# Optimization experiments

Measured on AMD Instinct MI355X. Metric: run time of the kernel, lower is better.

Reference implementation:

```python
import jax, jax.numpy as jnp
import numpy as np

B, N, DIM, H = 8, 1024, 1024, 16
D = DIM // H  # head dim = 64
SCALE = DIM ** (-0.5)  # NOTE: original uses full dim, not head dim


def setup_inputs() -> dict:
    key = jax.random.key(0)
    ks = jax.random.split(key, 8)
    x = jax.random.normal(ks[0], (B, N, DIM), dtype=jnp.float32)
    pos = jax.random.normal(ks[1], (B, N, DIM), dtype=jnp.float32)
    mask = jax.random.bernoulli(ks[2], 0.9, (B, N - 1))  # bool, [b, n-1]
    w_std = 0.02
    W_qk = jax.random.normal(ks[3], (2 * DIM, DIM), dtype=jnp.float32) * w_std  # Linear(dim, 2*dim_qk)
    W_v = jax.random.normal(ks[4], (DIM, DIM), dtype=jnp.float32) * w_std
    W_out = jax.random.normal(ks[5], (DIM, DIM), dtype=jnp.float32) * w_std
    b_out = jax.random.normal(ks[6], (DIM,), dtype=jnp.float32) * w_std
    return {"x": x, "mask": mask, "pos": pos, "W_qk": W_qk, "W_v": W_v,
            "W_out": W_out, "b_out": b_out}


def _split_heads(t):
    # b n (h d) -> b h n d
    b, n, _ = t.shape
    return t.reshape(b, n, H, D).transpose(0, 2, 1, 3)


def reference(x, mask, pos, W_qk, W_v, W_out, b_out):
    qk = x @ W_qk.T                       # [b, n, 2*dim]
    q, k = jnp.split(qk, 2, axis=-1)
    v = x @ W_v.T                         # [b, n, dim]
    q, k, v = _split_heads(q), _split_heads(k), _split_heads(v)  # [b,h,n,d]
    hpos = _split_heads(pos)
    q = q + hpos
    k = k + hpos
    dots = jnp.einsum('bhid,bhjd->bhij', q, k) * SCALE  # [b,h,n,n]
    mask_value = -jnp.finfo(dots.dtype).max
    # pad mask with True at position 0 (CLS token always visible)
    m = jnp.pad(mask, ((0, 0), (1, 0)), constant_values=True)  # [b, n]
    m2 = m[:, None, :] & m[:, :, None]                          # [b, n, n]
    dots = jnp.where(m2[:, None, :, :], dots, mask_value)
    attn = jax.nn.softmax(dots, axis=-1)
    out = jnp.einsum('bhij,bhjd->bhid', attn, v)  # [b,h,n,d]
    out = out.transpose(0, 2, 1, 3).reshape(x.shape[0], x.shape[1], DIM)  # b n (h d)
    out = out @ W_out.T + b_out  # dropout p=0.0 -> identity
    return out
```

## Files before the change

### kernel.cpp

```cpp
#include <hip/hip_runtime.h>


typedef unsigned short u16;
typedef short bf16x8 __attribute__((ext_vector_type(8)));
typedef float f32x4 __attribute__((ext_vector_type(4)));
typedef float f32x16 __attribute__((ext_vector_type(16)));

#define MFMA16(a, b, c) __builtin_amdgcn_mfma_f32_16x16x32_bf16((a), (b), (c), 0, 0, 0)
#define MFMA32(a, b, c) __builtin_amdgcn_mfma_f32_32x32x16_bf16((a), (b), (c), 0, 0, 0)

__device__ __forceinline__ u16 f2bf(float f) {
    union { float f; unsigned u; } x; x.f = f;
    unsigned r = x.u + 0x7fffu + ((x.u >> 16) & 1u);
    return (u16)(r >> 16);
}

__device__ __forceinline__ void gld16(const u16* g, u16* l) {
    __builtin_amdgcn_global_load_lds(
        (const __attribute__((address_space(1))) void*)g,
        (__attribute__((address_space(3))) void*)l, 16, 0, 0);
}

__global__ __launch_bounds__(256) void cast_f32_bf16(const float* __restrict__ src,
                                                     u16* __restrict__ dst, int n4) {
    int i = blockIdx.x * 256 + threadIdx.x;
    if (i < n4) {
        float4 v = ((const float4*)src)[i];
        ushort4 o;
        o.x = f2bf(v.x); o.y = f2bf(v.y); o.z = f2bf(v.z); o.w = f2bf(v.w);
        ((ushort4*)dst)[i] = o;
    }
}

__global__ __launch_bounds__(256) void gemm_qk(
    const u16* __restrict__ A,
    const u16* __restrict__ Bw,
    const float* __restrict__ pos,
    u16* __restrict__ Q, u16* __restrict__ Kx) {
    const int n0 = blockIdx.x * 128, m0 = blockIdx.y * 128;
    const int t = threadIdx.x, w = t >> 6, ln = t & 63;
    const int l15 = ln & 15, l4 = ln >> 4;
    const int wm = (w >> 1) * 64, wn = (w & 1) * 64;

    __shared__ u16 As[128 * 64];
    __shared__ u16 Bs[128 * 64];

    f32x4 acc[4][4];
#pragma unroll
    for (int i = 0; i < 4; ++i)
#pragma unroll
        for (int j = 0; j < 4; ++j) acc[i][j] = (f32x4){0.f, 0.f, 0.f, 0.f};

    const int sr = ln >> 3;
    const int scx = ((ln & 7) ^ sr) * 8;
    const int x0 = (l15 & 7);
    for (int k0 = 0; k0 < 1024; k0 += 64) {
        __syncthreads();
#pragma unroll
        for (int p = 0; p < 4; ++p) {
            int rbase = w * 32 + p * 8;
            gld16(A  + (size_t)(m0 + rbase + sr) * 1024 + k0 + scx, &As[rbase * 64]);
            gld16(Bw + (size_t)(n0 + rbase + sr) * 1024 + k0 + scx, &Bs[rbase * 64]);
        }
        __syncthreads();
#pragma unroll
        for (int kt = 0; kt < 2; ++kt) {
            bf16x8 a[4], bfr[4];
#pragma unroll
            for (int mt = 0; mt < 4; ++mt)
                a[mt] = *(const bf16x8*)&As[(wm + mt * 16 + l15) * 64 + ((kt * 4 + l4) ^ x0) * 8];
#pragma unroll
            for (int nt = 0; nt < 4; ++nt)
                bfr[nt] = *(const bf16x8*)&Bs[(wn + nt * 16 + l15) * 64 + ((kt * 4 + l4) ^ x0) * 8];
#pragma unroll
            for (int mt = 0; mt < 4; ++mt)
#pragma unroll
                for (int nt = 0; nt < 4; ++nt)
                    acc[mt][nt] = MFMA16(a[mt], bfr[nt], acc[mt][nt]);
        }
    }
#pragma unroll
    for (int mt = 0; mt < 4; ++mt)
#pragma unroll
        for (int nt = 0; nt < 4; ++nt)
#pragma unroll
            for (int r = 0; r < 4; ++r) {
                int i = m0 + wm + mt * 16 + l4 * 4 + r;
                int j = n0 + wn + nt * 16 + l15;
                int bb = i >> 10, n = i & 1023;
                int jj = j & 1023;
                float v = acc[mt][nt][r] + pos[(size_t)i * 1024 + jj];
                int hh = jj >> 6, dd = jj & 63;
                size_t idx = (((size_t)(bb * 16 + hh)) * 1024 + n) * 64 + dd;
                if (j < 1024) Q[idx] = f2bf(v * 0.045084220027780106f);
                else          Kx[idx] = f2bf(v);
            }
}

__global__ __launch_bounds__(256) void gemm_v(
    const u16* __restrict__ Wv,
    const u16* __restrict__ X,
    u16* __restrict__ Vt) {
    const int n0 = blockIdx.x * 128, m0 = blockIdx.y * 128;
    const int bIdx = blockIdx.z;
    const u16* Xb = X + (size_t)bIdx * 1048576;
    const int t = threadIdx.x, w = t >> 6, ln = t & 63;
    const int l15 = ln & 15, l4 = ln >> 4;
    const int wm = (w >> 1) * 64, wn = (w & 1) * 64;

    __shared__ u16 As[128 * 64];
    __shared__ u16 Bs[128 * 64];

    f32x4 acc[4][4];
#pragma unroll
    for (int i = 0; i < 4; ++i)
#pragma unroll
        for (int j = 0; j < 4; ++j) acc[i][j] = (f32x4){0.f, 0.f, 0.f, 0.f};

    const int sr = ln >> 3;
    const int scx = ((ln & 7) ^ sr) * 8;
    const int x0 = (l15 & 7);
    for (int k0 = 0; k0 < 1024; k0 += 64) {
        __syncthreads();
#pragma unroll
        for (int p = 0; p < 4; ++p) {
            int rbase = w * 32 + p * 8;
            gld16(Wv + (size_t)(m0 + rbase + sr) * 1024 + k0 + scx, &As[rbase * 64]);
            gld16(Xb + (size_t)(n0 + rbase + sr) * 1024 + k0 + scx, &Bs[rbase * 64]);
        }
        __syncthreads();
#pragma unroll
        for (int kt = 0; kt < 2; ++kt) {
            bf16x8 a[4], bfr[4];
#pragma unroll
            for (int mt = 0; mt < 4; ++mt)
                a[mt] = *(const bf16x8*)&As[(wm + mt * 16 + l15) * 64 + ((kt * 4 + l4) ^ x0) * 8];
#pragma unroll
            for (int nt = 0; nt < 4; ++nt)
                bfr[nt] = *(const bf16x8*)&Bs[(wn + nt * 16 + l15) * 64 + ((kt * 4 + l4) ^ x0) * 8];
#pragma unroll
            for (int mt = 0; mt < 4; ++mt)
#pragma unroll
                for (int nt = 0; nt < 4; ++nt)
                    acc[mt][nt] = MFMA16(a[mt], bfr[nt], acc[mt][nt]);
        }
    }
#pragma unroll
    for (int mt = 0; mt < 4; ++mt)
#pragma unroll
        for (int nt = 0; nt < 4; ++nt)
#pragma unroll
            for (int r = 0; r < 4; ++r) {
                int i = m0 + wm + mt * 16 + l4 * 4 + r;
                int j = n0 + wn + nt * 16 + l15;
                Vt[((size_t)(bIdx * 1024 + i)) * 1024 + j] = f2bf(acc[mt][nt][r]);
            }
}

__global__ __launch_bounds__(64) void vsum_kernel(const u16* __restrict__ Vt,
                                                  float* __restrict__ Vsum) {
    int row = blockIdx.x, ln = threadIdx.x;
    const u16* p = Vt + (size_t)row * 1024 + ln * 16;
    uint4 a = *(const uint4*)p;
    uint4 bq = *(const uint4*)(p + 8);
    float s = 0.f;
    unsigned vv[8] = {a.x, a.y, a.z, a.w, bq.x, bq.y, bq.z, bq.w};
#pragma unroll
    for (int i = 0; i < 8; ++i) {
        s += __uint_as_float(vv[i] << 16);
        s += __uint_as_float(vv[i] & 0xffff0000u);
    }
#pragma unroll
    for (int d = 1; d < 64; d <<= 1) s += __shfl_xor(s, d);
    if (ln == 0) Vsum[row] = s;
}

__global__ __launch_bounds__(256) void attn_kernel(
    const u16* __restrict__ Q,
    const u16* __restrict__ Kx,
    const u16* __restrict__ Vt,
    const int* __restrict__ maskIn,
    const float* __restrict__ Vsum,
    u16* __restrict__ O) {
    const int gid = blockIdx.x;
    const int bh = gid & 127;
    const int qt = gid >> 7;
    const int b = bh >> 4, h = bh & 15;
    const int t = threadIdx.x, w = t >> 6, ln = t & 63;
    const int l31 = ln & 31, l5 = ln >> 5;

    __shared__ u16 Ks[64 * 72];
    __shared__ u16 Vs[64 * 72];
    __shared__ float cvf[64];

    const size_t qkbase = (size_t)bh * 65536;
    const int q0 = qt * 128 + w * 32;
    const int q = q0 + l31;

    bf16x8 bq[4];
#pragma unroll
    for (int kt = 0; kt < 4; ++kt)
        bq[kt] = *(const bf16x8*)(Q + qkbase + (size_t)q * 64 + kt * 16 + l5 * 8);

    const bool rqv = (q == 0) || (maskIn[b * 1023 + q - 1] != 0);

    float lsum = 0.f;
    f32x16 o0 = {0,0,0,0,0,0,0,0,0,0,0,0,0,0,0,0};
    f32x16 o1 = {0,0,0,0,0,0,0,0,0,0,0,0,0,0,0,0};

    const int srow = t >> 2, sc = (t & 3) * 16;

    for (int j0 = 0; j0 < 1024; j0 += 64) {
        __syncthreads();
        {
            uint4 kv = *(const uint4*)(Kx + qkbase + (size_t)(j0 + srow) * 64 + sc);
            uint4 kv2 = *(const uint4*)(Kx + qkbase + (size_t)(j0 + srow) * 64 + sc + 8);
            *(uint4*)&Ks[srow * 72 + sc] = kv;
            *(uint4*)&Ks[srow * 72 + sc + 8] = kv2;
            uint4 vv = *(const uint4*)(Vt + (size_t)bh * 65536 + (size_t)srow * 1024 + j0 + sc);
            uint4 vv2 = *(const uint4*)(Vt + (size_t)bh * 65536 + (size_t)srow * 1024 + j0 + sc + 8);
            *(uint4*)&Vs[srow * 72 + sc] = vv;
            *(uint4*)&Vs[srow * 72 + sc + 8] = vv2;
            if (t < 64) {
                int kk = j0 + t;
                bool cv = (kk == 0) || (maskIn[b * 1023 + kk - 1] != 0);
                cvf[t] = cv ? 0.f : -1e30f;
            }
        }
        __syncthreads();

        f32x16 st0 = {0,0,0,0,0,0,0,0,0,0,0,0,0,0,0,0};
        f32x16 st1 = {0,0,0,0,0,0,0,0,0,0,0,0,0,0,0,0};
#pragma unroll
        for (int ktk = 0; ktk < 4; ++ktk) {
            bf16x8 ak0 = *(const bf16x8*)&Ks[(l31) * 72 + ktk * 16 + l5 * 8];
            bf16x8 ak1 = *(const bf16x8*)&Ks[(32 + l31) * 72 + ktk * 16 + l5 * 8];
            st0 = MFMA32(ak0, bq[ktk], st0);
            st1 = MFMA32(ak1, bq[ktk], st1);
        }
#pragma unroll
        for (int g = 0; g < 4; ++g) {
            f32x4 cv0 = *(const f32x4*)&cvf[g * 8 + l5 * 4];
            f32x4 cv1 = *(const f32x4*)&cvf[32 + g * 8 + l5 * 4];
#pragma unroll
            for (int r = 0; r < 4; ++r) {
                float p0 = __builtin_amdgcn_exp2f(st0[g * 4 + r] + cv0[r]);
                float p1 = __builtin_amdgcn_exp2f(st1[g * 4 + r] + cv1[r]);
                st0[g * 4 + r] = p0;
                st1[g * 4 + r] = p1;
                lsum += p0 + p1;
            }
        }
        unsigned pk0[8], pk1[8];
#pragma unroll
        for (int g = 0; g < 4; ++g) {
#pragma unroll
            for (int qq = 0; qq < 2; ++qq) {
                unsigned a0 = __float_as_uint(st0[g * 4 + 2 * qq]) + 0x8000u;
                unsigned a1 = __float_as_uint(st0[g * 4 + 2 * qq + 1]) + 0x8000u;
                pk0[2 * g + qq] = (a1 & 0xffff0000u) | (a0 >> 16);
                unsigned c0 = __float_as_uint(st1[g * 4 + 2 * qq]) + 0x8000u;
                unsigned c1 = __float_as_uint(st1[g * 4 + 2 * qq + 1]) + 0x8000u;
                pk1[2 * g + qq] = (c1 & 0xffff0000u) | (c0 >> 16);
            }
        }
        bf16x8 pf[4];
#pragma unroll
        for (int kt = 0; kt < 4; ++kt) {
            const int hh = kt & 1;
            unsigned own0, own1, off0, off1;
            if (kt < 2) {
                own0 = l5 ? pk0[4 * hh + 2] : pk0[4 * hh];
                own1 = l5 ? pk0[4 * hh + 3] : pk0[4 * hh + 1];
                off0 = l5 ? pk0[4 * hh]     : pk0[4 * hh + 2];
                off1 = l5 ? pk0[4 * hh + 1] : pk0[4 * hh + 3];
            } else {
                own0 = l5 ? pk1[4 * hh + 2] : pk1[4 * hh];
                own1 = l5 ? pk1[4 * hh + 3] : pk1[4 * hh + 1];
                off0 = l5 ? pk1[4 * hh]     : pk1[4 * hh + 2];
                off1 = l5 ? pk1[4 * hh + 1] : pk1[4 * hh + 3];
            }
            unsigned ex0 = (unsigned)__shfl_xor((int)off0, 32);
            unsigned ex1 = (unsigned)__shfl_xor((int)off1, 32);
            unsigned dw0 = l5 ? ex0 : own0;
            unsigned dw1 = l5 ? ex1 : own1;
            unsigned dw2 = l5 ? own0 : ex0;
            unsigned dw3 = l5 ? own1 : ex1;
            union { unsigned u[4]; bf16x8 v; } cv;
            cv.u[0] = dw0; cv.u[1] = dw1; cv.u[2] = dw2; cv.u[3] = dw3;
            pf[kt] = cv.v;
        }
#pragma unroll
        for (int kt = 0; kt < 4; ++kt) {
            bf16x8 av0 = *(const bf16x8*)&Vs[(l31) * 72 + kt * 16 + l5 * 8];
            bf16x8 av1 = *(const bf16x8*)&Vs[(32 + l31) * 72 + kt * 16 + l5 * 8];
            o0 = MFMA32(av0, pf[kt], o0);
            o1 = MFMA32(av1, pf[kt], o1);
        }
    }
    float lrow = lsum + __shfl_xor(lsum, 32);
    const float linv = 1.f / lrow;
    const int n = q0 + l31;
    u16* orow = O + ((size_t)(b * 1024 + n)) * 1024 + h * 64;
#pragma unroll
    for (int reg = 0; reg < 16; ++reg) {
        int d0 = (reg & 3) + 8 * (reg >> 2) + 4 * l5;
        float v0 = rqv ? o0[reg] * linv : Vsum[bh * 64 + d0] * 0.0009765625f;
        float v1 = rqv ? o1[reg] * linv : Vsum[bh * 64 + 32 + d0] * 0.0009765625f;
        orow[d0] = f2bf(v0);
        orow[32 + d0] = f2bf(v1);
    }
}

__global__ __launch_bounds__(256) void gemm_out(
    const u16* __restrict__ A,
    const u16* __restrict__ Bw,
    const float* __restrict__ bias,
    float* __restrict__ out) {
    const int n0 = blockIdx.x * 128, m0 = blockIdx.y * 128;
    const int t = threadIdx.x, w = t >> 6, ln = t & 63;
    const int l15 = ln & 15, l4 = ln >> 4;
    const int wm = (w >> 1) * 64, wn = (w & 1) * 64;

    __shared__ u16 As[128 * 64];
    __shared__ u16 Bs[128 * 64];

    f32x4 acc[4][4];
#pragma unroll
    for (int i = 0; i < 4; ++i)
#pragma unroll
        for (int j = 0; j < 4; ++j) acc[i][j] = (f32x4){0.f, 0.f, 0.f, 0.f};

    const int sr = ln >> 3;
    const int scx = ((ln & 7) ^ sr) * 8;
    const int x0 = (l15 & 7);
    for (int k0 = 0; k0 < 1024; k0 += 64) {
        __syncthreads();
#pragma unroll
        for (int p = 0; p < 4; ++p) {
            int rbase = w * 32 + p * 8;
            gld16(A  + (size_t)(m0 + rbase + sr) * 1024 + k0 + scx, &As[rbase * 64]);
            gld16(Bw + (size_t)(n0 + rbase + sr) * 1024 + k0 + scx, &Bs[rbase * 64]);
        }
        __syncthreads();
#pragma unroll
        for (int kt = 0; kt < 2; ++kt) {
            bf16x8 a[4], bfr[4];
#pragma unroll
            for (int mt = 0; mt < 4; ++mt)
                a[mt] = *(const bf16x8*)&As[(wm + mt * 16 + l15) * 64 + ((kt * 4 + l4) ^ x0) * 8];
#pragma unroll
            for (int nt = 0; nt < 4; ++nt)
                bfr[nt] = *(const bf16x8*)&Bs[(wn + nt * 16 + l15) * 64 + ((kt * 4 + l4) ^ x0) * 8];
#pragma unroll
            for (int mt = 0; mt < 4; ++mt)
#pragma unroll
                for (int nt = 0; nt < 4; ++nt)
                    acc[mt][nt] = MFMA16(a[mt], bfr[nt], acc[mt][nt]);
        }
    }
#pragma unroll
    for (int mt = 0; mt < 4; ++mt)
#pragma unroll
        for (int nt = 0; nt < 4; ++nt)
#pragma unroll
            for (int r = 0; r < 4; ++r) {
                int i = m0 + wm + mt * 16 + l4 * 4 + r;
                int j = n0 + wn + nt * 16 + l15;
                out[(size_t)i * 1024 + j] = acc[mt][nt][r] + bias[j];
            }
}

extern "C" void kernel_launch(void* const* d_in, const int* in_sizes, int n_in,
                              void* d_out, int out_size, void* d_ws, size_t ws_size,
                              hipStream_t stream) {
    const float* x    = (const float*)d_in[0];
    const int*   mask = (const int*)d_in[1];
    const float* pos  = (const float*)d_in[2];
    const float* wqk  = (const float*)d_in[3];
    const float* wv   = (const float*)d_in[4];
    const float* wout = (const float*)d_in[5];
    const float* bout = (const float*)d_in[6];

    char* ws = (char*)d_ws;
    u16* xbf    = (u16*)(ws + 0);
    u16* wqkvbf = (u16*)(ws + 16777216);
    u16* woutbf = (u16*)(ws + 23068672);
    u16* Qb     = (u16*)(ws + 25165824);
    u16* Kb     = (u16*)(ws + 41943040);
    u16* Vtb    = (u16*)(ws + 58720256);
    float* Vsum = (float*)(ws + 16777216);

    cast_f32_bf16<<<8192, 256, 0, stream>>>(x, xbf, 2097152);
    cast_f32_bf16<<<2048, 256, 0, stream>>>(wqk, wqkvbf, 524288);
    cast_f32_bf16<<<1024, 256, 0, stream>>>(wv, wqkvbf + 2097152, 262144);
    cast_f32_bf16<<<1024, 256, 0, stream>>>(wout, woutbf, 262144);

    gemm_qk<<<dim3(16, 64), 256, 0, stream>>>(xbf, wqkvbf, pos, Qb, Kb);
    gemm_v<<<dim3(8, 8, 8), 256, 0, stream>>>(wqkvbf + 2097152, xbf, Vtb);
    vsum_kernel<<<8192, 64, 0, stream>>>(Vtb, Vsum);
    attn_kernel<<<1024, 256, 0, stream>>>(Qb, Kb, Vtb, mask, Vsum, xbf);
    gemm_out<<<dim3(8, 64), 256, 0, stream>>>(xbf, woutbf, bout, (float*)d_out);
}
```

Before: 317.0 us.

## Split attention key range across two wave groups and fuse cast kernels

Attention blocks now hold 512 threads. Two halves each process half of the key sequence, and their partial outputs and row sums are combined through LDS at the end. The mask row is precomputed once into LDS instead of being loaded for every tile. The four f32-to-bf16 cast launches are merged into one kernel. Together these aim to raise parallelism per block and cut launch overhead, at the cost of more LDS use and an extra combine step with synchronisation.

After: 298.2 us. -5.9%, faster.

```diff
diff --git a/kernel.cpp b/kernel.cpp
--- a/kernel.cpp
+++ b/kernel.cpp
@@ -21,15 +21,20 @@
         (__attribute__((address_space(3))) void*)l, 16, 0, 0);
 }
 
-__global__ __launch_bounds__(256) void cast_f32_bf16(const float* __restrict__ src,
-                                                     u16* __restrict__ dst, int n4) {
+__global__ __launch_bounds__(256) void cast_all(
+    const float* __restrict__ x, const float* __restrict__ wqk,
+    const float* __restrict__ wv, const float* __restrict__ wout,
+    u16* __restrict__ xbf, u16* __restrict__ wqkvbf, u16* __restrict__ woutbf) {
     int i = blockIdx.x * 256 + threadIdx.x;
-    if (i < n4) {
-        float4 v = ((const float4*)src)[i];
-        ushort4 o;
-        o.x = f2bf(v.x); o.y = f2bf(v.y); o.z = f2bf(v.z); o.w = f2bf(v.w);
-        ((ushort4*)dst)[i] = o;
-    }
+    const float* src; u16* dst; int off;
+    if (i < 2097152)      { src = x;    dst = xbf;              off = i; }
+    else if (i < 2621440) { src = wqk;  dst = wqkvbf;           off = i - 2097152; }
+    else if (i < 2883584) { src = wv;   dst = wqkvbf + 2097152; off = i - 2621440; }
+    else                  { src = wout; dst = woutbf;           off = i - 2883584; }
+    float4 v = ((const float4*)src)[off];
+    ushort4 o;
+    o.x = f2bf(v.x); o.y = f2bf(v.y); o.z = f2bf(v.z); o.w = f2bf(v.w);
+    ((ushort4*)dst)[off] = o;
 }
 
 __global__ __launch_bounds__(256) void gemm_qk(
@@ -175,7 +180,7 @@
     if (ln == 0) Vsum[row] = s;
 }
 
-__global__ __launch_bounds__(256) void attn_kernel(
+__global__ __launch_bounds__(512) void attn_kernel(
     const u16* __restrict__ Q,
     const u16* __restrict__ Kx,
     const u16* __restrict__ Vt,
@@ -187,45 +192,46 @@
     const int qt = gid >> 7;
     const int b = bh >> 4, h = bh & 15;
     const int t = threadIdx.x, w = t >> 6, ln = t & 63;
+    const int half = w >> 2, wq = w & 3;
     const int l31 = ln & 31, l5 = ln >> 5;
 
-    __shared__ u16 Ks[64 * 72];
-    __shared__ u16 Vs[64 * 72];
-    __shared__ float cvf[64];
+    __shared__ __align__(16) char lds[40960];
+    u16* Ks = (u16*)(lds + half * 18432);
+    u16* Vs = (u16*)(lds + half * 18432 + 9216);
+    float* mch = (float*)(lds + 36864);
+
+    for (int i = t; i < 1024; i += 512)
+        mch[i] = (i == 0 || maskIn[b * 1023 + i - 1] != 0) ? 0.f : -1e30f;
 
     const size_t qkbase = (size_t)bh * 65536;
-    const int q0 = qt * 128 + w * 32;
+    const int q0 = qt * 128 + wq * 32;
     const int q = q0 + l31;
 
     bf16x8 bq[4];
 #pragma unroll
     for (int kt = 0; kt < 4; ++kt)
         bq[kt] = *(const bf16x8*)(Q + qkbase + (size_t)q * 64 + kt * 16 + l5 * 8);
-
-    const bool rqv = (q == 0) || (maskIn[b * 1023 + q - 1] != 0);
 
     float lsum = 0.f;
     f32x16 o0 = {0,0,0,0,0,0,0,0,0,0,0,0,0,0,0,0};
     f32x16 o1 = {0,0,0,0,0,0,0,0,0,0,0,0,0,0,0,0};
 
-    const int srow = t >> 2, sc = (t & 3) * 16;
-
-    for (int j0 = 0; j0 < 1024; j0 += 64) {
+    const int th = t & 255;
+    const int srow = th >> 2, sc = (th & 3) * 16;
+    const int jbase = half * 512;
+
+    for (int jt = 0; jt < 8; ++jt) {
+        const int j0 = jbase + jt * 64;
         __syncthreads();
         {
-            uint4 kv = *(const uint4*)(Kx + qkbase + (size_t)(j0 + srow) * 64 + sc);
+            uint4 kv  = *(const uint4*)(Kx + qkbase + (size_t)(j0 + srow) * 64 + sc);
             uint4 kv2 = *(const uint4*)(Kx + qkbase + (size_t)(j0 + srow) * 64 + sc + 8);
             *(uint4*)&Ks[srow * 72 + sc] = kv;
             *(uint4*)&Ks[srow * 72 + sc + 8] = kv2;
-            uint4 vv = *(const uint4*)(Vt + (size_t)bh * 65536 + (size_t)srow * 1024 + j0 + sc);
-            uint4 vv2 = *(const uint4*)(Vt + (size_t)bh * 65536 + (size_t)srow * 1024 + j0 + sc + 8);
+            uint4 vv  = *(const uint4*)(Vt + qkbase + (size_t)srow * 1024 + j0 + sc);
+            uint4 vv2 = *(const uint4*)(Vt + qkbase + (size_t)srow * 1024 + j0 + sc + 8);
             *(uint4*)&Vs[srow * 72 + sc] = vv;
             *(uint4*)&Vs[srow * 72 + sc + 8] = vv2;
-            if (t < 64) {
-                int kk = j0 + t;
-                bool cv = (kk == 0) || (maskIn[b * 1023 + kk - 1] != 0);
-                cvf[t] = cv ? 0.f : -1e30f;
-            }
         }
         __syncthreads();
 
@@ -240,8 +246,8 @@
         }
 #pragma unroll
         for (int g = 0; g < 4; ++g) {
-            f32x4 cv0 = *(const f32x4*)&cvf[g * 8 + l5 * 4];
-            f32x4 cv1 = *(const f32x4*)&cvf[32 + g * 8 + l5 * 4];
+            f32x4 cv0 = *(const f32x4*)&mch[j0 + g * 8 + l5 * 4];
+            f32x4 cv1 = *(const f32x4*)&mch[j0 + 32 + g * 8 + l5 * 4];
 #pragma unroll
             for (int r = 0; r < 4; ++r) {
                 float p0 = __builtin_amdgcn_exp2f(st0[g * 4 + r] + cv0[r]);
@@ -298,17 +304,33 @@
             o1 = MFMA32(av1, pf[kt], o1);
         }
     }
-    float lrow = lsum + __shfl_xor(lsum, 32);
-    const float linv = 1.f / lrow;
-    const int n = q0 + l31;
-    u16* orow = O + ((size_t)(b * 1024 + n)) * 1024 + h * 64;
-#pragma unroll
-    for (int reg = 0; reg < 16; ++reg) {
-        int d0 = (reg & 3) + 8 * (reg >> 2) + 4 * l5;
-        float v0 = rqv ? o0[reg] * linv : Vsum[bh * 64 + d0] * 0.0009765625f;
-        float v1 = rqv ? o1[reg] * linv : Vsum[bh * 64 + 32 + d0] * 0.0009765625f;
-        orow[d0] = f2bf(v0);
-        orow[32 + d0] = f2bf(v1);
+    __syncthreads();
+    float* comb = (float*)lds;
+    if (half == 1) {
+        float* dst = comb + ((size_t)(wq * 64 + ln)) * 33;
+#pragma unroll
+        for (int i = 0; i < 16; ++i) { dst[i] = o0[i]; dst[16 + i] = o1[i]; }
+        dst[32] = lsum;
+    }
+    __syncthreads();
+    if (half == 0) {
+        const float* src = comb + ((size_t)(wq * 64 + ln)) * 33;
+#pragma unroll
+        for (int i = 0; i < 16; ++i) { o0[i] += src[i]; o1[i] += src[16 + i]; }
+        lsum += src[32];
+        float lrow = lsum + __shfl_xor(lsum, 32);
+        const float linv = 1.f / lrow;
+        const bool rqv = (mch[q] == 0.f);
+        const int n = q0 + l31;
+        u16* orow = O + ((size_t)(b * 1024 + n)) * 1024 + h * 64;
+#pragma unroll
+        for (int reg = 0; reg < 16; ++reg) {
+            int d0 = (reg & 3) + 8 * (reg >> 2) + 4 * l5;
+            float v0 = rqv ? o0[reg] * linv : Vsum[bh * 64 + d0] * 0.0009765625f;
+            float v1 = rqv ? o1[reg] * linv : Vsum[bh * 64 + 32 + d0] * 0.0009765625f;
+            orow[d0] = f2bf(v0);
+            orow[32 + d0] = f2bf(v1);
+        }
     }
 }
 
@@ -391,14 +413,11 @@
     u16* Vtb    = (u16*)(ws + 58720256);
     float* Vsum = (float*)(ws + 16777216);
 
-    cast_f32_bf16<<<8192, 256, 0, stream>>>(x, xbf, 2097152);
-    cast_f32_bf16<<<2048, 256, 0, stream>>>(wqk, wqkvbf, 524288);
-    cast_f32_bf16<<<1024, 256, 0, stream>>>(wv, wqkvbf + 2097152, 262144);
-    cast_f32_bf16<<<1024, 256, 0, stream>>>(wout, woutbf, 262144);
+    cast_all<<<12288, 256, 0, stream>>>(x, wqk, wv, wout, xbf, wqkvbf, woutbf);
 
     gemm_qk<<<dim3(16, 64), 256, 0, stream>>>(xbf, wqkvbf, pos, Qb, Kb);
     gemm_v<<<dim3(8, 8, 8), 256, 0, stream>>>(wqkvbf + 2097152, xbf, Vtb);
     vsum_kernel<<<8192, 64, 0, stream>>>(Vtb, Vsum);
-    attn_kernel<<<1024, 256, 0, stream>>>(Qb, Kb, Vtb, mask, Vsum, xbf);
+    attn_kernel<<<1024, 512, 0, stream>>>(Qb, Kb, Vtb, mask, Vsum, xbf);
     gemm_out<<<dim3(8, 64), 256, 0, stream>>>(xbf, woutbf, bout, (float*)d_out);
 }
```
